# Kernel optimization log

Hardware: AMD Instinct MI355X
Metric: run time of the kernel (lower is better)

## Reference

```python
import jax, jax.numpy as jnp
import numpy as np

B, T, D = 1, 1024, 1024
H = 16; HKV = 16; HD = D // H; R = 2; K = 3; LOWR = 32
HR = HKV * R                      # heads after harmonic expansion
OUTW = HKV * HD * 2 * R           # w_proj output width
SCALE = HD ** -0.5


def setup_inputs() -> dict:
    key = jax.random.key(0)
    ks = jax.random.split(key, 10)
    def rn(k, shape, sc=1.0):
        return jax.random.normal(k, shape, dtype=jnp.float32) * sc
    return {
        'hidden_states': rn(ks[0], (B, T, D)),
        'q_w': rn(ks[1], (D, D), D ** -0.5),
        'k_w': rn(ks[2], (D, D), D ** -0.5),
        'v_w': rn(ks[3], (D, D), D ** -0.5),
        'w1': rn(ks[4], (LOWR, D), D ** -0.5),
        'w2': rn(ks[5], (OUTW, LOWR), LOWR ** -0.5),
        'conv_w': rn(ks[6], (OUTW, K), K ** -0.5),
        'bt_w': rn(ks[7], (HKV * R, D), D ** -0.5),
        'bt_b': jnp.zeros((HKV * R,), jnp.float32),
        'o_w': rn(ks[8], (D, D * R), (D * R) ** -0.5),
        'omega': 0.01 * jnp.ones((1, 1, 1, R), jnp.float32),
        'phi': jnp.zeros((1, 1, 1, R), jnp.float32),
    }


def path_attention_forward(hidden_states, q_w, k_w, v_w, w1, w2, conv_w,
                           bt_w, bt_b, o_w, omega, phi):
    b, t, _ = hidden_states.shape
    q = hidden_states @ q_w.T
    k = hidden_states @ k_w.T
    v = hidden_states @ v_w.T
    # low-rank w projection, causal depthwise short conv (kernel K), SiLU
    w_raw = (hidden_states @ w1.T) @ w2.T                    # [b,t,OUTW]
    xp = jnp.pad(w_raw, ((0, 0), (K - 1, 0), (0, 0)))
    w_raw = sum(xp[:, i:i + t, :] * conv_w[:, i] for i in range(K))
    w_raw = jax.nn.silu(w_raw)
    # rotary-like harmonic mixing of Householder directions
    w5 = w_raw.reshape(b, t, HKV, 2 * R, HD)
    Ah = w5[:, :, :, 0::2, :]                                # [b,t,HKV,R,HD]
    Bh = w5[:, :, :, 1::2, :]
    pos = jnp.arange(t, dtype=jnp.float32)[None, :, None, None]
    theta = omega * pos + phi                                # [1,t,1,R]
    c = jnp.cos(theta)[..., None]
    s = jnp.sin(theta)[..., None]
    Wdir = Ah * c + Bh * s
    Wdir = Wdir * jax.lax.rsqrt(jnp.sum(Wdir * Wdir, -1, keepdims=True) + 1e-6)
    beta = jax.nn.sigmoid(hidden_states @ bt_w.T + bt_b) * 2.0   # [b,t,HR]
    # repeat-interleave q/k/v heads across harmonics -> [b,HR,t,HD]
    to_h = lambda x: jnp.swapaxes(jnp.repeat(x.reshape(b, t, H, HD), R, axis=2), 1, 2)
    qh, kh, vh = to_h(q), to_h(k), to_h(v)
    wh = jnp.swapaxes(Wdir.reshape(b, t, HR, HD), 1, 2)      # [b,HR,t,HD]
    bh = jnp.swapaxes(beta, 1, 2)                            # [b,HR,t]
    # PaTH logits: A_ij = q_i^T (H_i ... H_{j+1}) k_j, H_t = I - beta_t w_t w_t^T.
    # WY/UT transform: with M_ts = beta_t (w_t.w_s) for s<t, the coefficients
    # B_tj (t>j) of the accumulated rank-1 corrections solve the unit-lower
    # triangular system (I + M) B = strilow(Db W K^T), and
    # A = tril(Q K^T - tril(Q W^T) B).
    idx = jnp.arange(t)
    strict = idx[:, None] > idx[None, :]
    incl = idx[:, None] >= idx[None, :]
    Mw = jnp.where(strict, jnp.einsum('bhtd,bhsd->bhts', wh, wh) * bh[..., None], 0.0)
    rhs = jnp.where(strict, jnp.einsum('bhtd,bhjd->bhtj', wh, kh) * bh[..., None], 0.0)
    Bmat = jax.scipy.linalg.solve_triangular(Mw + jnp.eye(t, dtype=Mw.dtype), rhs, lower=True)
    qk = jnp.einsum('bhid,bhjd->bhij', qh, kh)
    qw = jnp.where(incl, jnp.einsum('bhid,bhtd->bhit', qh, wh), 0.0)
    logits = (qk - jnp.einsum('bhit,bhtj->bhij', qw, Bmat)) * SCALE
    logits = jnp.where(incl, logits, -1e30)
    p = jax.nn.softmax(logits, axis=-1)
    o = jnp.einsum('bhij,bhjd->bhid', p, vh)                 # [b,HR,t,HD]
    o = jnp.swapaxes(o, 1, 2).reshape(b, t, HR * HD)         # [b,t,D*R]
    return o @ o_w.T


def reference(hidden_states, q_w, k_w, v_w, w1, w2, conv_w, bt_w, bt_b, o_w, omega, phi):
    return path_attention_forward(hidden_states, q_w, k_w, v_w, w1, w2, conv_w,
                                  bt_w, bt_b, o_w, omega, phi)
```

## Files before the change

kernel.cpp:

```cpp
#include <hip/hip_runtime.h>
#include <math.h>

#define TTD 1024
#define DDM 1024
#define HDIM 64
#define PSCALE 0.125f
#define PSC2 0.18033688011112042f
#define LS 72

typedef __attribute__((ext_vector_type(8))) __bf16 bf16x8;
typedef __attribute__((ext_vector_type(4))) float f32x4;
#define MFMA16(a,b,c) __builtin_amdgcn_mfma_f32_16x16x32_bf16(a,b,c,0,0,0)

#define STR_(x) #x
#define WAITVM(N) asm volatile("s_waitcnt vmcnt(" STR_(N) ")" ::: "memory")
#define BAR() do { __builtin_amdgcn_s_barrier(); asm volatile("" ::: "memory"); } while (0)
#define LGKBAR() do { asm volatile("s_waitcnt lgkmcnt(0)" ::: "memory"); \
                      __builtin_amdgcn_s_barrier(); asm volatile("" ::: "memory"); } while (0)
#define FULLBAR() do { asm volatile("s_waitcnt vmcnt(0) lgkmcnt(0)" ::: "memory"); \
                       __builtin_amdgcn_s_barrier(); asm volatile("" ::: "memory"); } while (0)

__device__ __forceinline__ ushort f2b(float f) {
  unsigned u = __builtin_bit_cast(unsigned, f);
  return (ushort)((u + 0x7fffu + ((u >> 16) & 1u)) >> 16);
}
__device__ __forceinline__ float b2f(ushort u) {
  unsigned v = (unsigned)u << 16;
  return __builtin_bit_cast(float, v);
}

__device__ __forceinline__ void gload_lds16(const ushort* g, ushort* l) {
  __builtin_amdgcn_global_load_lds(
      (const __attribute__((address_space(1))) unsigned*)g,
      (__attribute__((address_space(3))) unsigned*)l, 16, 0, 0);
}

#define SWZ(row, cc) (((row) * 8 + ((cc) ^ ((row) & 7))) * 8)
#define SWZE(row, col) (SWZ(row, (col) >> 3) + ((col) & 7))

__device__ __forceinline__ void stage_tile(const ushort* gb, long gs, ushort* tile,
                                           int w, int l) {
  int sub = l >> 3, cc = (l & 7) ^ sub;
  #pragma unroll
  for (int it = 0; it < 2; ++it) {
    int q = w * 2 + it;
    gload_lds16(gb + (long)(q * 8 + sub) * gs + cc * 8, &tile[(q * 64 + l) * 8]);
  }
}

__device__ __forceinline__ bf16x8 frag(const ushort* tile, int row, int cc) {
  return *(const bf16x8*)&tile[SWZ(row, cc)];
}

#define XT_PERH   557056L
#define OFF_X     0L
#define OFF_PZ    35651584L
#define OFF_HSB   35651584L
#define OFF_QWW   37748736L
#define OFF_KWW   39845888L
#define OFF_VWW   41943040L
#define OFF_W2B   44040192L
#define OFF_WLOWB 44302336L
#define OFF_TB    98566144L
#define OFF_OALL  98566144L
#define OFF_YB    102760448L
#define OFF_OWB   106954752L
#define OFF_WHB   111149056L
#define OFF_QB    115343360L
#define OFF_KB    117440512L
#define OFF_VTB   119537664L
#define OFF_BETA  121634816L
#define OFF_BW64  121765888L

#define CVT_TOTAL 6488064L
struct CvtSegs {
  const float* src[8];
  ushort* dst[8];
  long cnt[8];
};
__global__ __launch_bounds__(256) void cvt_all_kernel(CvtSegs sg) {
  long e = ((long)blockIdx.x * 256 + threadIdx.x) * 4;
  #pragma unroll
  for (int s = 0; s < 8; ++s) {
    if (e < sg.cnt[s]) {
      float4 f = *(const float4*)(sg.src[s] + e);
      ushort4 o;
      o.x = f2b(f.x); o.y = f2b(f.y); o.z = f2b(f.z); o.w = f2b(f.w);
      *(ushort4*)(sg.dst[s] + e) = o;
      return;
    }
    e -= sg.cnt[s];
  }
}

__global__ __launch_bounds__(256) void qkv_sp_kernel(
    const ushort* __restrict__ hsb,
    const ushort* __restrict__ wq, const ushort* __restrict__ wk, const ushort* __restrict__ wv,
    const ushort* __restrict__ bw, const float* __restrict__ bt_b,
    ushort* __restrict__ cq, ushort* __restrict__ ck, ushort* __restrict__ cv,
    float* __restrict__ beta, ushort* __restrict__ wlowb)
{
  int z = blockIdx.z;
  if (z == 3 && blockIdx.x != 0) return;
  const ushort* B = (z == 0) ? wq : (z == 1) ? wk : (z == 2) ? wv : bw;

  __shared__ ushort Ab[2][8192];
  __shared__ ushort Bb[2][4096];

  int tid = threadIdx.x, w = tid >> 6, l = tid & 63;
  int quad = l >> 4, lane15 = l & 15;
  int rm = blockIdx.y * 128, cn = (z == 3) ? 0 : blockIdx.x * 64;
  const ushort* Ag = hsb + (long)rm * DDM;
  const ushort* Bg = B + (long)cn * DDM;

  stage_tile(Ag, DDM, &Ab[0][0], w, l);
  stage_tile(Ag + 64 * DDM, DDM, &Ab[0][4096], w, l);
  stage_tile(Bg, DDM, &Bb[0][0], w, l);

  f32x4 acc[2][4] = {};
  int arow0 = (w & 1) * 32 + lane15;
  int asel = (w >> 1) * 4096;
  for (int kt = 0; kt < 16; ++kt) {
    int cur = kt & 1;
    if (kt < 15) {
      int nxt = cur ^ 1;
      stage_tile(Ag + (kt + 1) * 64, DDM, &Ab[nxt][0], w, l);
      stage_tile(Ag + 64 * DDM + (kt + 1) * 64, DDM, &Ab[nxt][4096], w, l);
      stage_tile(Bg + (kt + 1) * 64, DDM, &Bb[nxt][0], w, l);
      WAITVM(6);
    } else {
      WAITVM(0);
    }
    BAR();
    const ushort* Atile = &Ab[cur][asel];
    #pragma unroll
    for (int s = 0; s < 2; ++s) {
      bf16x8 a0 = frag(Atile, arow0, s * 4 + quad);
      bf16x8 a1 = frag(Atile, arow0 + 16, s * 4 + quad);
      #pragma unroll
      for (int f = 0; f < 4; ++f) {
        bf16x8 bf = frag(&Bb[cur][0], f * 16 + lane15, s * 4 + quad);
        acc[0][f] = MFMA16(a0, bf, acc[0][f]);
        acc[1][f] = MFMA16(a1, bf, acc[1][f]);
      }
    }
    BAR();
  }

  if (z < 2) {
    ushort* Cb = (z == 0) ? cq : ck;
    #pragma unroll
    for (int rr = 0; rr < 2; ++rr) {
      int orow = rm + w * 32 + rr * 16 + quad * 4;
      #pragma unroll
      for (int f = 0; f < 4; ++f)
        #pragma unroll
        for (int r = 0; r < 4; ++r)
          Cb[(long)(orow + r) * DDM + cn + f * 16 + lane15] = f2b(acc[rr][f][r]);
    }
  } else if (z == 2) {
    #pragma unroll
    for (int rr = 0; rr < 2; ++rr) {
      int orow = rm + w * 32 + rr * 16 + quad * 4;
      #pragma unroll
      for (int f = 0; f < 4; ++f) {
        ushort4 o;
        o.x = f2b(acc[rr][f][0]); o.y = f2b(acc[rr][f][1]);
        o.z = f2b(acc[rr][f][2]); o.w = f2b(acc[rr][f][3]);
        *(ushort4*)&cv[(long)(cn + f * 16 + lane15) * TTD + orow] = o;
      }
    }
  } else {
    #pragma unroll
    for (int rr = 0; rr < 2; ++rr) {
      int orow = rm + w * 32 + rr * 16 + quad * 4;
      #pragma unroll
      for (int f = 0; f < 2; ++f) {
        int hr = f * 16 + lane15;
        float bb = bt_b[hr];
        #pragma unroll
        for (int r = 0; r < 4; ++r)
          beta[(long)hr * TTD + orow + r] = 2.f / (1.f + expf(-(acc[rr][f][r] + bb)));
      }
      #pragma unroll
      for (int f = 2; f < 4; ++f)
        #pragma unroll
        for (int r = 0; r < 4; ++r)
          wlowb[(long)(orow + r) * 32 + (f - 2) * 16 + lane15] = f2b(acc[rr][f][r]);
    }
  }
}

__global__ __launch_bounds__(256) void wraw_solveA_kernel(
    const ushort* __restrict__ wlowb, const ushort* __restrict__ w2b,
    const float* __restrict__ conv_w, const float* __restrict__ omega,
    const float* __restrict__ phi, const float* __restrict__ beta,
    ushort* __restrict__ whb, ushort* __restrict__ TB, ushort* __restrict__ YB)
{
  int c = blockIdx.x;
  int rm = c * 64;
  int p = blockIdx.y;
  int hkv = p >> 1, r = p & 1;
  int c0 = hkv * 256 + r * 128;

  __shared__ char pool_[65568];
  ushort* As = (ushort*)pool_;
  ushort* Bs = (ushort*)(pool_ + 4096);
  float (*WR)[132] = (float(*)[132])(pool_ + 12288);
  ushort* Wrow = (ushort*)(pool_ + 47136);
  ushort* WT   = (ushort*)(pool_ + 56352);
  float (*Lm)[65] = (float(*)[65])pool_;
  float (*Vf)[65] = (float(*)[65])(pool_ + 16640);
  ushort* Tb = (ushort*)(pool_ + 33280);

  int tid = threadIdx.x, w = tid >> 6, l = tid & 63;
  int quad = l >> 4, lane15 = l & 15;

  {
    int row = tid >> 2, ch = (tid & 3) * 8;
    gload_lds16(wlowb + (long)(rm + row) * 32 + ch, &As[row * 32 + ch]);
    gload_lds16(w2b + (long)(c0 + row) * 32 + ch, &Bs[row * 32 + ch]);
    gload_lds16(w2b + (long)(c0 + 64 + row) * 32 + ch, &Bs[(64 + row) * 32 + ch]);
  }
  {
    int hr2 = tid >> 7, col = tid & 127;
    float acc = 0.f;
    if (rm > 0) {
      long t = rm - 2 + hr2;
      for (int k = 0; k < 32; ++k)
        acc += b2f(wlowb[t * 32 + k]) * b2f(w2b[(long)(c0 + col) * 32 + k]);
    }
    WR[hr2][col] = acc;
  }
  FULLBAR();

  #pragma unroll
  for (int g = 0; g < 2; ++g) {
    f32x4 acc[4] = {};
    bf16x8 af = *(const bf16x8*)&As[(w * 16 + lane15) * 32 + quad * 8];
    #pragma unroll
    for (int f = 0; f < 4; ++f) {
      bf16x8 bf = *(const bf16x8*)&Bs[(g * 64 + f * 16 + lane15) * 32 + quad * 8];
      acc[f] = MFMA16(af, bf, acc[f]);
    }
    #pragma unroll
    for (int f = 0; f < 4; ++f)
      #pragma unroll
      for (int rr = 0; rr < 4; ++rr)
        WR[2 + w * 16 + quad * 4 + rr][g * 64 + f * 16 + lane15] = acc[f][rr];
  }
  LGKBAR();

  {
    float cwa[3], cwb[3];
    #pragma unroll
    for (int i = 0; i < 3; ++i) {
      cwa[i] = conv_w[(long)(c0 + l) * 3 + i];
      cwb[i] = conv_w[(long)(c0 + 64 + l) * 3 + i];
    }
    float om = omega[r], ph = phi[r];
    for (int it = 0; it < 16; ++it) {
      int tl = it * 4 + w;
      int t = rm + tl;
      float a = cwa[0] * WR[tl][l] + cwa[1] * WR[tl + 1][l] + cwa[2] * WR[tl + 2][l];
      float b = cwb[0] * WR[tl][64 + l] + cwb[1] * WR[tl + 1][64 + l] + cwb[2] * WR[tl + 2][64 + l];
      a = a / (1.f + expf(-a));
      b = b / (1.f + expf(-b));
      float th = om * (float)t + ph;
      float wd = a * cosf(th) + b * sinf(th);
      float ss = wd * wd;
      #pragma unroll
      for (int o = 32; o > 0; o >>= 1) ss += __shfl_xor(ss, o, 64);
      ushort hv = f2b(wd * (1.f / sqrtf(ss + 1e-6f)));
      whb[((long)p * TTD + t) * HDIM + l] = hv;
      Wrow[tl * LS + l] = hv;
      WT[l * LS + tl] = hv;
    }
  }
  LGKBAR();

  const float* bet = beta + (long)p * TTD + rm;
  ushort* TBh = TB + ((long)p * 16 + c) * 4096;
  ushort* YBh = YB + ((long)p * 16 + c) * 4096;

  f32x4 g4[4] = {};
  #pragma unroll
  for (int s = 0; s < 2; ++s) {
    bf16x8 af = *(const bf16x8*)&Wrow[(w * 16 + lane15) * LS + s * 32 + quad * 8];
    #pragma unroll
    for (int f = 0; f < 4; ++f) {
      bf16x8 bf = *(const bf16x8*)&Wrow[(f * 16 + lane15) * LS + s * 32 + quad * 8];
      g4[f] = MFMA16(af, bf, g4[f]);
    }
  }
  #pragma unroll
  for (int r4 = 0; r4 < 4; ++r4) {
    int t = w * 16 + quad * 4 + r4;
    float bv = bet[t];
    #pragma unroll
    for (int f = 0; f < 4; ++f) {
      int tp = f * 16 + lane15;
      Lm[t][tp] = (t > tp) ? bv * g4[f][r4] : 0.f;
    }
  }
  LGKBAR();

  {
    float cur[16];
    #pragma unroll
    for (int i = 0; i < 16; ++i) cur[i] = (w * 16 + i == l) ? bet[l] : 0.f;
    for (int sb = 0; sb < 4; ++sb) {
      if (w == sb) {
        float xloc[16];
        #pragma unroll
        for (int i = 0; i < 16; ++i) {
          float bv = cur[i];
          #pragma unroll
          for (int j2 = 0; j2 < 16; ++j2)
            if (j2 < i) bv -= Lm[sb * 16 + i][sb * 16 + j2] * xloc[j2];
          xloc[i] = bv;
          Vf[sb * 16 + i][l] = bv;
        }
      }
      LGKBAR();
      if (w > sb) {
        float xp[16];
        #pragma unroll
        for (int t = 0; t < 16; ++t) xp[t] = Vf[sb * 16 + t][l];
        #pragma unroll
        for (int i = 0; i < 16; ++i) {
          float s2 = cur[i];
          #pragma unroll
          for (int t = 0; t < 16; ++t) s2 -= Lm[w * 16 + i][sb * 16 + t] * xp[t];
          cur[i] = s2;
        }
      }
    }
  }
  {
    int t = tid >> 2, off = (tid & 3) * 16;
    ushort tmp[16];
    #pragma unroll
    for (int i = 0; i < 16; ++i) { tmp[i] = f2b(Vf[t][off + i]); Tb[t * LS + off + i] = tmp[i]; }
    *(uint4*)&TBh[t * 64 + off] = *(const uint4*)&tmp[0];
    *(uint4*)&TBh[t * 64 + off + 8] = *(const uint4*)&tmp[8];
  }
  LGKBAR();
  f32x4 y[4] = {};
  #pragma unroll
  for (int s = 0; s < 2; ++s) {
    bf16x8 af = *(const bf16x8*)&Tb[(w * 16 + lane15) * LS + s * 32 + quad * 8];
    #pragma unroll
    for (int f = 0; f < 4; ++f) {
      bf16x8 bf = *(const bf16x8*)&WT[(f * 16 + lane15) * LS + s * 32 + quad * 8];
      y[f] = MFMA16(af, bf, y[f]);
    }
  }
  #pragma unroll
  for (int f = 0; f < 4; ++f)
    #pragma unroll
    for (int r4 = 0; r4 < 4; ++r4)
      YBh[(long)(w * 16 + quad * 4 + r4) * 64 + f * 16 + lane15] = f2b(y[f][r4]);
}

__global__ __launch_bounds__(256) void solveB_kernel(
    const ushort* __restrict__ whb, const ushort* __restrict__ kb,
    const ushort* __restrict__ TB, const ushort* __restrict__ YB,
    ushort* __restrict__ Xb, ushort* __restrict__ KZ)
{
  int h = blockIdx.x;
  int ty = blockIdx.y;
  int js = (ty < 8) ? ty : (23 - ty);
  int j0 = js * 64;
  const ushort* wh_h = whb + (long)h * TTD * HDIM;
  const ushort* k_h = kb + (long)(h >> 1) * 64;
  ushort* X_h = Xb + (long)h * XT_PERH;
  ushort* KZ_h = KZ + (long)h * 15 * TTD * HDIM;
  int xidx = js * 16 - js * (js - 1) / 2;

  __shared__ ushort KT[4096];
  __shared__ ushort WT[4096];
  __shared__ ushort XM[4096];
  __shared__ ushort nS[4096];

  int tid = threadIdx.x, w = tid >> 6, l = tid & 63;
  int quad = l >> 4, lane15 = l & 15;
  f32x4 Sacc[4] = {}, Wacc[4] = {};

  stage_tile(k_h + (long)j0 * DDM, DDM, KT, w, l);

  float kreg[4][4];
  #pragma unroll
  for (int f = 0; f < 4; ++f)
    #pragma unroll
    for (int r = 0; r < 4; ++r)
      kreg[f][r] = b2f(k_h[(long)(j0 + w * 16 + quad * 4 + r) * DDM + f * 16 + lane15]);

  WAITVM(0);

  for (int c = js; c < 16; ++c) {
    const ushort* whc = wh_h + (long)c * 64 * HDIM;
    LGKBAR();
    {
      int d0 = (tid & 7) * 8;
      #pragma unroll
      for (int it = 0; it < 2; ++it) {
        int t = it * 32 + (tid >> 3);
        uint4 pk = *(const uint4*)&whc[(long)t * HDIM + d0];
        const ushort* pu = (const ushort*)&pk;
        #pragma unroll
        for (int i = 0; i < 8; ++i) WT[SWZE(d0 + i, t)] = pu[i];
      }
    }
    f32x4 xacc[4] = {};
    if (c == js) {
      f32x4 m[4] = {};
      #pragma unroll
      for (int s = 0; s < 2; ++s) {
        bf16x8 af = *(const bf16x8*)&whc[(long)(w * 16 + lane15) * HDIM + s * 32 + quad * 8];
        #pragma unroll
        for (int f = 0; f < 4; ++f)
          m[f] = MFMA16(af, frag(KT, f * 16 + lane15, s * 4 + quad), m[f]);
      }
      #pragma unroll
      for (int f = 0; f < 4; ++f)
        #pragma unroll
        for (int r = 0; r < 4; ++r) {
          int t = w * 16 + quad * 4 + r, j = f * 16 + lane15;
          XM[SWZE(j, t)] = (t > j) ? f2b(m[f][r]) : (ushort)0;
        }
      LGKBAR();
      const ushort* TBh = TB + ((long)h * 16 + c) * 4096;
      #pragma unroll
      for (int s = 0; s < 2; ++s) {
        bf16x8 af = *(const bf16x8*)&TBh[(long)(w * 16 + lane15) * 64 + s * 32 + quad * 8];
        #pragma unroll
        for (int f = 0; f < 4; ++f)
          xacc[f] = MFMA16(af, frag(XM, f * 16 + lane15, s * 4 + quad), xacc[f]);
      }
      LGKBAR();
    } else {
      const ushort* YBh = YB + ((long)h * 16 + c) * 4096;
      #pragma unroll
      for (int s = 0; s < 2; ++s) {
        bf16x8 af = *(const bf16x8*)&YBh[(long)(w * 16 + lane15) * 64 + s * 32 + quad * 8];
        #pragma unroll
        for (int f = 0; f < 4; ++f) {
          xacc[f] = MFMA16(af, frag(KT, f * 16 + lane15, s * 4 + quad), xacc[f]);
          xacc[f] = MFMA16(af, frag(nS, f * 16 + lane15, s * 4 + quad), xacc[f]);
        }
      }
    }
    #pragma unroll
    for (int f = 0; f < 4; ++f)
      #pragma unroll
      for (int r = 0; r < 4; ++r)
        XM[SWZE(f * 16 + lane15, w * 16 + quad * 4 + r)] = f2b(xacc[f][r]);
    LGKBAR();
    {
      ushort* xt = X_h + (long)xidx * 4096;
      int j = tid >> 2, c2 = (tid & 3) * 2;
      bf16x8 s0 = frag(XM, j, c2);
      bf16x8 s1 = frag(XM, j, c2 + 1);
      *(bf16x8*)&xt[j * 64 + c2 * 8] = s0;
      *(bf16x8*)&xt[j * 64 + c2 * 8 + 8] = s1;
    }
    ++xidx;
    if (c < 15) {
      #pragma unroll
      for (int s = 0; s < 2; ++s) {
        bf16x8 aw = frag(WT, w * 16 + lane15, s * 4 + quad);
        bf16x8 ax = frag(XM, w * 16 + lane15, s * 4 + quad);
        #pragma unroll
        for (int f = 0; f < 4; ++f) {
          Sacc[f] = MFMA16(aw, frag(XM, f * 16 + lane15, s * 4 + quad), Sacc[f]);
          Wacc[f] = MFMA16(ax, frag(WT, f * 16 + lane15, s * 4 + quad), Wacc[f]);
        }
      }
      ushort* pz = KZ_h + (long)c * TTD * HDIM;
      #pragma unroll
      for (int f = 0; f < 4; ++f)
        #pragma unroll
        for (int r = 0; r < 4; ++r)
          pz[(long)(j0 + w * 16 + quad * 4 + r) * 64 + f * 16 + lane15] =
              f2b(kreg[f][r] - Wacc[f][r]);
      #pragma unroll
      for (int f = 0; f < 4; ++f)
        #pragma unroll
        for (int r = 0; r < 4; ++r)
          nS[SWZE(f * 16 + lane15, w * 16 + quad * 4 + r)] = f2b(-Sacc[f][r]);
    }
  }
}

__global__ __launch_bounds__(256) void flash_kernel(
    const ushort* __restrict__ qb, const ushort* __restrict__ kbuf,
    const ushort* __restrict__ whb, const ushort* __restrict__ Xb,
    const ushort* __restrict__ KZ, const ushort* __restrict__ vTb,
    ushort* __restrict__ oall)
{
  int h = blockIdx.x;
  int y = blockIdx.y;
  int ri = (y < 8) ? y : (23 - y);
  int r0 = ri * 64;
  const ushort* q_h = qb + (long)(h >> 1) * 64;
  const ushort* k_h = kbuf + (long)(h >> 1) * 64;
  const ushort* wh_h = whb + (long)h * TTD * HDIM;
  const ushort* X_h = Xb + (long)h * XT_PERH;
  const ushort* kz = KZ + ((long)h * 15 + (ri - 1)) * TTD * HDIM;
  const ushort* v_h = vTb + (long)(h >> 1) * 64 * TTD;

  __shared__ ushort S[2][3][4096];
  __shared__ ushort KD[4096];
  __shared__ ushort QWD[4096];
  __shared__ ushort PT[4096];

  int tid = threadIdx.x, w = tid >> 6, l = tid & 63;
  int quad = l >> 4, lane15 = l & 15;

  bf16x8 aq[2];
  #pragma unroll
  for (int s = 0; s < 2; ++s)
    aq[s] = *(const bf16x8*)&q_h[(long)(r0 + w * 16 + lane15) * DDM + s * 32 + quad * 8];
  const ushort* xst = X_h + (long)ri * 4096;
  stage_tile(k_h + (long)r0 * DDM, DDM, KD, w, l);
  if (ri > 0) stage_tile(kz, 64, &S[0][0][0], w, l);
  stage_tile(xst, 64, &S[0][1][0], w, l);
  stage_tile(v_h, TTD, &S[0][2][0], w, l);
  {
    f32x4 t4[4] = {};
    #pragma unroll
    for (int s = 0; s < 2; ++s)
      #pragma unroll
      for (int f = 0; f < 4; ++f) {
        bf16x8 bf = *(const bf16x8*)&wh_h[(long)(r0 + f * 16 + lane15) * HDIM + s * 32 + quad * 8];
        t4[f] = MFMA16(aq[s], bf, t4[f]);
      }
    #pragma unroll
    for (int f = 0; f < 4; ++f)
      #pragma unroll
      for (int r = 0; r < 4; ++r) {
        int i = w * 16 + quad * 4 + r, t = f * 16 + lane15;
        QWD[SWZE(i, t)] = (i >= t) ? f2b(-t4[f][r]) : (ushort)0;
      }
  }

  f32x4 O[4] = {};
  float m[4], lsum[4];
  #pragma unroll
  for (int r = 0; r < 4; ++r) { m[r] = -1e30f; lsum[r] = 0.f; }

  for (int jb = 0; jb <= ri; ++jb) {
    int cur = jb & 1;
    const ushort* xnx = xst + (long)(15 - jb) * 4096;
    if (jb < ri) {
      long c0n = (long)(jb + 1) * 64;
      ushort* nb = &S[cur ^ 1][0][0];
      if (jb + 1 < ri) {
        stage_tile(kz + c0n * 64, 64, nb, w, l);
        stage_tile(xnx, 64, nb + 4096, w, l);
        stage_tile(v_h + c0n, TTD, nb + 8192, w, l);
        WAITVM(6);
      } else {
        stage_tile(xnx, 64, nb + 4096, w, l);
        stage_tile(v_h + c0n, TTD, nb + 8192, w, l);
        WAITVM(4);
      }
    } else {
      WAITVM(0);
    }
    BAR();
    const ushort* Skz = &S[cur][0][0];
    const ushort* Sx  = &S[cur][1][0];
    const ushort* Sv  = &S[cur][2][0];
    f32x4 acc[4] = {};
    const ushort* Sb = (jb < ri) ? Skz : KD;
    #pragma unroll
    for (int s = 0; s < 2; ++s)
      #pragma unroll
      for (int f = 0; f < 4; ++f)
        acc[f] = MFMA16(aq[s], frag(Sb, f * 16 + lane15, s * 4 + quad), acc[f]);
    #pragma unroll
    for (int s = 0; s < 2; ++s) {
      bf16x8 aw = frag(QWD, w * 16 + lane15, s * 4 + quad);
      #pragma unroll
      for (int f = 0; f < 4; ++f)
        acc[f] = MFMA16(aw, frag(Sx, f * 16 + lane15, s * 4 + quad), acc[f]);
    }
    float rmax[4] = {-3e38f, -3e38f, -3e38f, -3e38f};
    #pragma unroll
    for (int f = 0; f < 4; ++f)
      #pragma unroll
      for (int r = 0; r < 4; ++r) {
        float lv = acc[f][r] * PSC2;
        if (jb == ri && (f * 16 + lane15) > (w * 16 + quad * 4 + r)) lv = -3e38f;
        acc[f][r] = lv;
        rmax[r] = fmaxf(rmax[r], lv);
      }
    #pragma unroll
    for (int r = 0; r < 4; ++r) {
      rmax[r] = fmaxf(rmax[r], __shfl_xor(rmax[r], 1, 64));
      rmax[r] = fmaxf(rmax[r], __shfl_xor(rmax[r], 2, 64));
      rmax[r] = fmaxf(rmax[r], __shfl_xor(rmax[r], 4, 64));
      rmax[r] = fmaxf(rmax[r], __shfl_xor(rmax[r], 8, 64));
    }
    float alpha[4], rs[4] = {0.f, 0.f, 0.f, 0.f};
    #pragma unroll
    for (int r = 0; r < 4; ++r) {
      float nm = fmaxf(m[r], rmax[r]);
      alpha[r] = exp2f(m[r] - nm);
      m[r] = nm;
    }
    #pragma unroll
    for (int f = 0; f < 4; ++f)
      #pragma unroll
      for (int r = 0; r < 4; ++r) {
        float e = exp2f(acc[f][r] - m[r]);
        acc[f][r] = e;
        rs[r] += e;
      }
    #pragma unroll
    for (int r = 0; r < 4; ++r) {
      rs[r] += __shfl_xor(rs[r], 1, 64);
      rs[r] += __shfl_xor(rs[r], 2, 64);
      rs[r] += __shfl_xor(rs[r], 4, 64);
      rs[r] += __shfl_xor(rs[r], 8, 64);
      lsum[r] = lsum[r] * alpha[r] + rs[r];
    }
    #pragma unroll
    for (int f = 0; f < 4; ++f)
      #pragma unroll
      for (int r = 0; r < 4; ++r) O[f][r] *= alpha[r];
    #pragma unroll
    for (int f = 0; f < 4; ++f)
      #pragma unroll
      for (int r = 0; r < 4; ++r) {
        int i = w * 16 + quad * 4 + r;
        PT[SWZE(i, f * 16 + lane15)] = f2b(acc[f][r]);
      }
    #pragma unroll
    for (int s = 0; s < 2; ++s) {
      bf16x8 ap = frag(PT, w * 16 + lane15, s * 4 + quad);
      #pragma unroll
      for (int f = 0; f < 4; ++f)
        O[f] = MFMA16(ap, frag(Sv, f * 16 + lane15, s * 4 + quad), O[f]);
    }
    BAR();
    xst = xnx;
  }
  #pragma unroll
  for (int r = 0; r < 4; ++r) lsum[r] = 1.f / lsum[r];
  #pragma unroll
  for (int f = 0; f < 4; ++f)
    #pragma unroll
    for (int r = 0; r < 4; ++r)
      oall[(long)(r0 + w * 16 + quad * 4 + r) * 2048 + h * 64 + f * 16 + lane15] =
          f2b(O[f][r] * lsum[r]);
}

__global__ __launch_bounds__(256) void gemm_out_kernel(
    const ushort* __restrict__ A, const ushort* __restrict__ Bb, float* __restrict__ C)
{
  __shared__ ushort Ab[2][8192];
  __shared__ ushort Bt[2][8192];
  int tid = threadIdx.x, w = tid >> 6, l = tid & 63;
  int quad = l >> 4, lane15 = l & 15;
  int rm = blockIdx.y * 64, cn = blockIdx.x * 64;
  const ushort* Ag = A + (long)rm * 2048;
  const ushort* Bg = Bb + (long)cn * 2048;

  stage_tile(Ag, 2048, &Ab[0][0], w, l);
  stage_tile(Ag + 64, 2048, &Ab[0][4096], w, l);
  stage_tile(Bg, 2048, &Bt[0][0], w, l);
  stage_tile(Bg + 64, 2048, &Bt[0][4096], w, l);

  f32x4 acc[4] = {};
  for (int kt = 0; kt < 16; ++kt) {
    int cur = kt & 1;
    if (kt < 15) {
      int nxt = cur ^ 1;
      long o = (long)(kt + 1) * 128;
      stage_tile(Ag + o, 2048, &Ab[nxt][0], w, l);
      stage_tile(Ag + o + 64, 2048, &Ab[nxt][4096], w, l);
      stage_tile(Bg + o, 2048, &Bt[nxt][0], w, l);
      stage_tile(Bg + o + 64, 2048, &Bt[nxt][4096], w, l);
      WAITVM(8);
    } else {
      WAITVM(0);
    }
    BAR();
    #pragma unroll
    for (int u = 0; u < 2; ++u)
      #pragma unroll
      for (int s = 0; s < 2; ++s) {
        bf16x8 af = frag(&Ab[cur][u * 4096], w * 16 + lane15, s * 4 + quad);
        #pragma unroll
        for (int f = 0; f < 4; ++f)
          acc[f] = MFMA16(af, frag(&Bt[cur][u * 4096], f * 16 + lane15, s * 4 + quad), acc[f]);
      }
    BAR();
  }
  int orow = rm + w * 16 + quad * 4;
  #pragma unroll
  for (int f = 0; f < 4; ++f)
    #pragma unroll
    for (int r = 0; r < 4; ++r)
      C[(long)(orow + r) * DDM + cn + f * 16 + lane15] = acc[f][r];
}

extern "C" void kernel_launch(void* const* d_in, const int* in_sizes, int n_in,
                              void* d_out, int out_size, void* d_ws, size_t ws_size,
                              hipStream_t stream) {
  const float* hs     = (const float*)d_in[0];
  const float* q_w    = (const float*)d_in[1];
  const float* k_w    = (const float*)d_in[2];
  const float* v_w    = (const float*)d_in[3];
  const float* w1     = (const float*)d_in[4];
  const float* w2     = (const float*)d_in[5];
  const float* conv_w = (const float*)d_in[6];
  const float* bt_w   = (const float*)d_in[7];
  const float* bt_b   = (const float*)d_in[8];
  const float* o_w    = (const float*)d_in[9];
  const float* omega  = (const float*)d_in[10];
  const float* phi    = (const float*)d_in[11];
  float* out = (float*)d_out;
  char* ws = (char*)d_ws;

  ushort* Xb     = (ushort*)(ws + OFF_X);
  ushort* KZb    = (ushort*)(ws + OFF_PZ);
  ushort* hs_b   = (ushort*)(ws + OFF_HSB);
  ushort* qw_wb  = (ushort*)(ws + OFF_QWW);
  ushort* kw_wb  = (ushort*)(ws + OFF_KWW);
  ushort* vw_wb  = (ushort*)(ws + OFF_VWW);
  ushort* w2_b   = (ushort*)(ws + OFF_W2B);
  ushort* wlow_b = (ushort*)(ws + OFF_WLOWB);
  ushort* TB     = (ushort*)(ws + OFF_TB);
  ushort* o_all  = (ushort*)(ws + OFF_OALL);
  ushort* YB     = (ushort*)(ws + OFF_YB);
  ushort* ow_b   = (ushort*)(ws + OFF_OWB);
  ushort* wh_b   = (ushort*)(ws + OFF_WHB);
  ushort* q_b    = (ushort*)(ws + OFF_QB);
  ushort* k_b    = (ushort*)(ws + OFF_KB);
  ushort* vT_b   = (ushort*)(ws + OFF_VTB);
  float*  beta   = (float*)(ws + OFF_BETA);
  ushort* bw_b   = (ushort*)(ws + OFF_BW64);

  CvtSegs sg;
  sg.src[0] = hs;   sg.dst[0] = hs_b;          sg.cnt[0] = 1048576;
  sg.src[1] = q_w;  sg.dst[1] = qw_wb;         sg.cnt[1] = 1048576;
  sg.src[2] = k_w;  sg.dst[2] = kw_wb;         sg.cnt[2] = 1048576;
  sg.src[3] = v_w;  sg.dst[3] = vw_wb;         sg.cnt[3] = 1048576;
  sg.src[4] = w2;   sg.dst[4] = w2_b;          sg.cnt[4] = 131072;
  sg.src[5] = bt_w; sg.dst[5] = bw_b;          sg.cnt[5] = 32768;
  sg.src[6] = w1;   sg.dst[6] = bw_b + 32768;  sg.cnt[6] = 32768;
  sg.src[7] = o_w;  sg.dst[7] = ow_b;          sg.cnt[7] = 2097152;
  cvt_all_kernel<<<dim3((CVT_TOTAL + 1023) / 1024), 256, 0, stream>>>(sg);

  qkv_sp_kernel<<<dim3(16, 8, 4), 256, 0, stream>>>(
      hs_b, qw_wb, kw_wb, vw_wb, bw_b, bt_b, q_b, k_b, vT_b, beta, wlow_b);

  wraw_solveA_kernel<<<dim3(16, 32), 256, 0, stream>>>(
      wlow_b, w2_b, conv_w, omega, phi, beta, wh_b, TB, YB);

  solveB_kernel<<<dim3(32, 16), 256, 0, stream>>>(wh_b, k_b, TB, YB, Xb, KZb);

  flash_kernel<<<dim3(32, 16), 256, 0, stream>>>(q_b, k_b, wh_b, Xb, KZb, vT_b, o_all);

  gemm_out_kernel<<<dim3(16, 16), 256, 0, stream>>>(o_all, ow_b, out);

  (void)in_sizes; (void)n_in; (void)out_size; (void)ws_size;
}
```

Before: 224.0 us.

## Prefetch next chunk's W and Y tiles into registers and reswizzle WT

In the per-chunk loop of the path-attention kernel, the global loads of the next chunk's W rows and Y fragments are issued one iteration early into registers, so their latency overlaps the current chunk's MFMA work. It also adds a second XOR swizzle (row>>3 folded in) for the transposed WT tile to reduce LDS bank conflicts on the scattered transpose writes. This costs extra registers, which may lower occupancy.

Measured after the change: 213.2 us. 1.05x faster.

```diff
diff --git a/kernel.cpp b/kernel.cpp
--- a/kernel.cpp
+++ b/kernel.cpp
@@ -37,6 +37,8 @@
 
 #define SWZ(row, cc) (((row) * 8 + ((cc) ^ ((row) & 7))) * 8)
 #define SWZE(row, col) (SWZ(row, (col) >> 3) + ((col) & 7))
+#define SWZ2(row, cc) (((row) * 8 + ((cc) ^ (((row) & 7) ^ ((row) >> 3)))) * 8)
+#define SWZ2E(row, col) (SWZ2(row, (col) >> 3) + ((col) & 7))
 
 __device__ __forceinline__ void stage_tile(const ushort* gb, long gs, ushort* tile,
                                            int w, int l) {
@@ -50,6 +52,9 @@
 
 __device__ __forceinline__ bf16x8 frag(const ushort* tile, int row, int cc) {
   return *(const bf16x8*)&tile[SWZ(row, cc)];
+}
+__device__ __forceinline__ bf16x8 frag2(const ushort* tile, int row, int cc) {
+  return *(const bf16x8*)&tile[SWZ2(row, cc)];
 }
 
 #define XT_PERH   557056L
@@ -396,24 +401,30 @@
     for (int r = 0; r < 4; ++r)
       kreg[f][r] = b2f(k_h[(long)(j0 + w * 16 + quad * 4 + r) * DDM + f * 16 + lane15]);
 
+  int prow0 = tid >> 3, pd0 = (tid & 7) * 8;
+  uint4 pk0 = *(const uint4*)&wh_h[((long)js * 64 + prow0) * HDIM + pd0];
+  uint4 pk1 = *(const uint4*)&wh_h[((long)js * 64 + 32 + prow0) * HDIM + pd0];
+  bf16x8 ybr0 = {}, ybr1 = {};
+
   WAITVM(0);
 
   for (int c = js; c < 16; ++c) {
-    const ushort* whc = wh_h + (long)c * 64 * HDIM;
     LGKBAR();
     {
-      int d0 = (tid & 7) * 8;
-      #pragma unroll
-      for (int it = 0; it < 2; ++it) {
-        int t = it * 32 + (tid >> 3);
-        uint4 pk = *(const uint4*)&whc[(long)t * HDIM + d0];
-        const ushort* pu = (const ushort*)&pk;
-        #pragma unroll
-        for (int i = 0; i < 8; ++i) WT[SWZE(d0 + i, t)] = pu[i];
-      }
+      const ushort* pu0 = (const ushort*)&pk0;
+      const ushort* pu1 = (const ushort*)&pk1;
+      #pragma unroll
+      for (int i = 0; i < 8; ++i) WT[SWZ2E(pd0 + i, prow0)] = pu0[i];
+      #pragma unroll
+      for (int i = 0; i < 8; ++i) WT[SWZ2E(pd0 + i, 32 + prow0)] = pu1[i];
+    }
+    if (c < 15) {
+      pk0 = *(const uint4*)&wh_h[((long)(c + 1) * 64 + prow0) * HDIM + pd0];
+      pk1 = *(const uint4*)&wh_h[((long)(c + 1) * 64 + 32 + prow0) * HDIM + pd0];
     }
     f32x4 xacc[4] = {};
     if (c == js) {
+      const ushort* whc = wh_h + (long)c * 64 * HDIM;
       f32x4 m[4] = {};
       #pragma unroll
       for (int s = 0; s < 2; ++s) {
@@ -440,15 +451,12 @@
       }
       LGKBAR();
     } else {
-      const ushort* YBh = YB + ((long)h * 16 + c) * 4096;
-      #pragma unroll
-      for (int s = 0; s < 2; ++s) {
-        bf16x8 af = *(const bf16x8*)&YBh[(long)(w * 16 + lane15) * 64 + s * 32 + quad * 8];
-        #pragma unroll
-        for (int f = 0; f < 4; ++f) {
-          xacc[f] = MFMA16(af, frag(KT, f * 16 + lane15, s * 4 + quad), xacc[f]);
-          xacc[f] = MFMA16(af, frag(nS, f * 16 + lane15, s * 4 + quad), xacc[f]);
-        }
+      #pragma unroll
+      for (int f = 0; f < 4; ++f) {
+        xacc[f] = MFMA16(ybr0, frag(KT, f * 16 + lane15, 0 * 4 + quad), xacc[f]);
+        xacc[f] = MFMA16(ybr0, frag(nS, f * 16 + lane15, 0 * 4 + quad), xacc[f]);
+        xacc[f] = MFMA16(ybr1, frag(KT, f * 16 + lane15, 1 * 4 + quad), xacc[f]);
+        xacc[f] = MFMA16(ybr1, frag(nS, f * 16 + lane15, 1 * 4 + quad), xacc[f]);
       }
     }
     #pragma unroll
@@ -467,14 +475,19 @@
     }
     ++xidx;
     if (c < 15) {
+      {
+        const ushort* YBn = YB + ((long)h * 16 + c + 1) * 4096;
+        ybr0 = *(const bf16x8*)&YBn[(long)(w * 16 + lane15) * 64 + 0 * 32 + quad * 8];
+        ybr1 = *(const bf16x8*)&YBn[(long)(w * 16 + lane15) * 64 + 1 * 32 + quad * 8];
+      }
       #pragma unroll
       for (int s = 0; s < 2; ++s) {
-        bf16x8 aw = frag(WT, w * 16 + lane15, s * 4 + quad);
+        bf16x8 aw = frag2(WT, w * 16 + lane15, s * 4 + quad);
         bf16x8 ax = frag(XM, w * 16 + lane15, s * 4 + quad);
         #pragma unroll
         for (int f = 0; f < 4; ++f) {
           Sacc[f] = MFMA16(aw, frag(XM, f * 16 + lane15, s * 4 + quad), Sacc[f]);
-          Wacc[f] = MFMA16(ax, frag(WT, f * 16 + lane15, s * 4 + quad), Wacc[f]);
+          Wacc[f] = MFMA16(ax, frag2(WT, f * 16 + lane15, s * 4 + quad), Wacc[f]);
         }
       }
       ushort* pz = KZ_h + (long)c * TTD * HDIM;
```
